# Optimization experiments

Measured on AMD Instinct MI355X. Metric: run time of the kernel, lower is better.

Reference implementation:

```python
import jax, jax.numpy as jnp
import numpy as np

EPS = 1e-5  # batchnorm eps (torch default)


def setup_inputs() -> dict:
    key = jax.random.key(0)
    ks = jax.random.split(key, 16)
    N, E, Din, H, Dout = 100000, 600000, 128, 128, 64
    x = jax.random.normal(ks[0], (N, Din), dtype=jnp.float32)
    edge_index = jax.random.randint(ks[1], (2, E), 0, N, dtype=jnp.int64)
    def lin(k, fan_in, fan_out):
        s = 1.0 / np.sqrt(fan_in)
        return jax.random.uniform(k, (fan_in, fan_out), jnp.float32, -s, s)
    return {
        "x": x,
        "edge_index": edge_index,
        "W1": lin(ks[2], Din, H), "b1": jnp.zeros((H,), jnp.float32),
        "W2": lin(ks[3], H, H),   "b2": jnp.zeros((H,), jnp.float32),
        "W3": lin(ks[4], H, H),   "b3": jnp.zeros((H,), jnp.float32),
        "W4": lin(ks[5], H, Dout),"b4": jnp.zeros((Dout,), jnp.float32),
        "g1": jnp.ones((H,), jnp.float32), "be1": jnp.zeros((H,), jnp.float32),
        "g2": jnp.ones((H,), jnp.float32), "be2": jnp.zeros((H,), jnp.float32),
        "g3": jnp.ones((H,), jnp.float32), "be3": jnp.zeros((H,), jnp.float32),
    }


def _gcn_norm(edge_index, N, dtype):
    # GCNConv default: add self-loops, symmetric normalization D^-1/2 A D^-1/2
    loop = jnp.arange(N, dtype=edge_index.dtype)
    src = jnp.concatenate([edge_index[0], loop])
    dst = jnp.concatenate([edge_index[1], loop])
    deg = jax.ops.segment_sum(jnp.ones_like(src, dtype=dtype), dst, num_segments=N)
    dinv = jax.lax.rsqrt(deg)  # deg >= 1 thanks to self-loops
    norm = dinv[src] * dinv[dst]  # [E+N]
    return src, dst, norm


def _conv(h, W, b, src, dst, norm, N):
    hw = h @ W                      # [N, out]
    msg = hw[src] * norm[:, None]   # gather + scale, [E+N, out]
    return jax.ops.segment_sum(msg, dst, num_segments=N) + b


def _bn(h, gamma, beta):
    # training-mode batchnorm over node dimension (biased variance)
    mu = jnp.mean(h, axis=0)
    var = jnp.mean(jnp.square(h - mu), axis=0)
    return (h - mu) * jax.lax.rsqrt(var + EPS) * gamma + beta


def reference(x, edge_index, W1, b1, W2, b2, W3, b3, W4, b4,
              g1, be1, g2, be2, g3, be3):
    N = x.shape[0]
    src, dst, norm = _gcn_norm(edge_index, N, x.dtype)
    h = jax.nn.relu(_conv(x, W1, b1, src, dst, norm, N))
    h = _bn(h, g1, be1)
    h = jax.nn.relu(_conv(h, W2, b2, src, dst, norm, N))
    h = _bn(h, g2, be2)
    h = jax.nn.relu(_conv(h, W3, b3, src, dst, norm, N))
    h = _bn(h, g3, be3)
    h = jax.nn.relu(_conv(h, W4, b4, src, dst, norm, N))
    return h
```

## Files before the change

kernel.cpp:

```cpp
#include <hip/hip_runtime.h>

#define BN_EPS 1e-5f

using bfrag = __attribute__((ext_vector_type(8))) short;
using f32x4 = __attribute__((ext_vector_type(4))) float;

__device__ inline float bf2f(unsigned int h16) {
    union { unsigned int u; float f; } v; v.u = h16 << 16; return v.f;
}
__device__ inline unsigned short f2bf(float f) {
    union { float f; unsigned int u; } v; v.f = f;
    unsigned int u = v.u;
    u += 0x7fffu + ((u >> 16) & 1u);
    return (unsigned short)(u >> 16);
}
__device__ inline void unpack8(uint4 u, float* f) {
    f[0] = bf2f(u.x & 0xffffu); f[1] = bf2f(u.x >> 16);
    f[2] = bf2f(u.y & 0xffffu); f[3] = bf2f(u.y >> 16);
    f[4] = bf2f(u.z & 0xffffu); f[5] = bf2f(u.z >> 16);
    f[6] = bf2f(u.w & 0xffffu); f[7] = bf2f(u.w >> 16);
}


__global__ void count_kernel(const int* __restrict__ ei, int E, int* __restrict__ cnt) {
    int e = blockIdx.x * blockDim.x + threadIdx.x;
    if (e < E) atomicAdd(&cnt[ei[E + e]], 1);
}

__global__ void dinv_kernel(const int* __restrict__ cnt, float* __restrict__ dinv, int N) {
    int i = blockIdx.x * blockDim.x + threadIdx.x;
    if (i < N) dinv[i] = rsqrtf((float)(cnt[i] + 1));
}

__global__ __launch_bounds__(1024) void scan_blocks(const int* __restrict__ cnt,
                                                    int* __restrict__ rowptr,
                                                    int* __restrict__ bsum, int N) {
    __shared__ int sh[1024];
    int t = threadIdx.x;
    int i = blockIdx.x * 1024 + t;
    int v = (i < N) ? cnt[i] : 0;
    sh[t] = v;
    __syncthreads();
    for (int off = 1; off < 1024; off <<= 1) {
        int x = (t >= off) ? sh[t - off] : 0;
        __syncthreads();
        sh[t] += x;
        __syncthreads();
    }
    if (i < N) rowptr[i] = sh[t] - v;
    if (t == 1023) bsum[blockIdx.x] = sh[1023];
}

__global__ void scan_carry(const int* __restrict__ bsum, int* __restrict__ boff, int nblk) {
    if (threadIdx.x == 0 && blockIdx.x == 0) {
        int run = 0;
        for (int b = 0; b < nblk; ++b) { int v = bsum[b]; boff[b] = run; run += v; }
        boff[nblk] = run;
    }
}

__global__ void scan_add(int* __restrict__ rowptr, const int* __restrict__ boff,
                         int* __restrict__ cursor, int N, int nblk) {
    int i = blockIdx.x * blockDim.x + threadIdx.x;
    if (i < N) {
        int v = rowptr[i] + boff[i >> 10];
        rowptr[i] = v;
        cursor[i] = v;
    }
    if (i == 0) rowptr[N] = boff[nblk];
}

__global__ void fill_kernel(const int* __restrict__ ei, int E, int* __restrict__ cursor,
                            const float* __restrict__ dinv, int* __restrict__ eidx,
                            float* __restrict__ enorm) {
    int e = blockIdx.x * blockDim.x + threadIdx.x;
    if (e < E) {
        int s = ei[e], d = ei[E + e];
        int p = atomicAdd(&cursor[d], 1);
        eidx[p]  = s;
        enorm[p] = dinv[s] * dinv[d];
    }
}

__global__ void s_kernel(const int* __restrict__ rowptr, const float* __restrict__ enorm,
                         const float* __restrict__ dinv, float* __restrict__ sarr, int N) {
    int i = blockIdx.x * blockDim.x + threadIdx.x;
    if (i < N) {
        float a = dinv[i] * dinv[i];
        int j1 = rowptr[i + 1];
        for (int j = rowptr[i]; j < j1; ++j) a += enorm[j];
        sarr[i] = a;
    }
}


template <bool HASBN>
__global__ __launch_bounds__(256) void prep_kernel(const float* __restrict__ W, int COLS,
                                                   const float* __restrict__ stats,
                                                   const float* __restrict__ g,
                                                   const float* __restrict__ be, float invN,
                                                   unsigned short* __restrict__ Wt,
                                                   float* __restrict__ cvec) {
    __shared__ float sc[128], sh[128];
    int tid = threadIdx.x;
    if (tid < 128) {
        if (HASBN) {
            float mu  = stats[tid] * invN;
            float var = stats[128 + tid] * invN - mu * mu;
            float rs  = rsqrtf(var + BN_EPS);
            float s   = rs * g[tid];
            sc[tid] = s;
            sh[tid] = be[tid] - mu * s;
        } else { sc[tid] = 1.f; sh[tid] = 0.f; }
    }
    __syncthreads();
    int total = 128 * COLS;
    for (int idx = blockIdx.x * 256 + tid; idx < total; idx += gridDim.x * 256) {
        int k = idx / COLS, j = idx % COLS;
        Wt[j * 128 + k] = f2bf(sc[k] * W[idx]);
    }
    if (blockIdx.x == 0 && tid < COLS) {
        float a = 0.f;
        if (HASBN)
            for (int k = 0; k < 128; ++k) a += sh[k] * W[k * COLS + tid];
        cvec[tid] = a;
    }
}


template <int COLS, bool IN_F32>
__global__ __launch_bounds__(256) void gemm_mfma(const void* __restrict__ Hin,
                                                 const unsigned short* __restrict__ Wt,
                                                 unsigned short* __restrict__ out, int N) {
    __shared__ unsigned short Hs[64][136];
    const int tid  = threadIdx.x;
    const int row0 = blockIdx.x * 64;

    if (IN_F32) {
        const float* H = (const float*)Hin;
#pragma unroll
        for (int it = 0; it < 8; ++it) {
            int idx = it * 256 + tid;
            int r = idx >> 5, c4 = (idx & 31) * 4;
            float4 v = {0.f, 0.f, 0.f, 0.f};
            if (row0 + r < N) v = *(const float4*)(H + (size_t)(row0 + r) * 128 + c4);
            Hs[r][c4 + 0] = f2bf(v.x); Hs[r][c4 + 1] = f2bf(v.y);
            Hs[r][c4 + 2] = f2bf(v.z); Hs[r][c4 + 3] = f2bf(v.w);
        }
    } else {
        const unsigned short* H = (const unsigned short*)Hin;
#pragma unroll
        for (int it = 0; it < 4; ++it) {
            int idx = it * 256 + tid;
            int r = idx >> 4, c8 = (idx & 15) * 8;
            uint4 v = {0u, 0u, 0u, 0u};
            if (row0 + r < N) v = *(const uint4*)(H + (size_t)(row0 + r) * 128 + c8);
            *(uint4*)&Hs[r][c8] = v;
        }
    }
    __syncthreads();

    const int lane = tid & 63, wave = tid >> 6;
    const int arow = lane & 15, kg = lane >> 4;
    const int r0   = wave * 16;

    bfrag af[4];
#pragma unroll
    for (int kc = 0; kc < 4; ++kc) af[kc] = *(const bfrag*)&Hs[r0 + arow][kc * 32 + kg * 8];

    constexpr int NT = COLS / 16;
    f32x4 acc[NT];
#pragma unroll
    for (int nt = 0; nt < NT; ++nt) acc[nt] = (f32x4){0.f, 0.f, 0.f, 0.f};

#pragma unroll
    for (int nt = 0; nt < NT; ++nt) {
        const unsigned short* wp = Wt + (size_t)(nt * 16 + arow) * 128 + kg * 8;
#pragma unroll
        for (int kc = 0; kc < 4; ++kc) {
            bfrag bf = *(const bfrag*)(wp + kc * 32);
            acc[nt] = __builtin_amdgcn_mfma_f32_16x16x32_bf16(af[kc], bf, acc[nt], 0, 0, 0);
        }
    }
    __syncthreads();

#pragma unroll
    for (int nt = 0; nt < NT; ++nt) {
        int col = nt * 16 + arow;
#pragma unroll
        for (int r = 0; r < 4; ++r)
            Hs[r0 + kg * 4 + r][col] = f2bf(acc[nt][r]);
    }
    __syncthreads();

    constexpr int CH = COLS / 8;
    for (int idx = tid; idx < 64 * CH; idx += 256) {
        int r = idx / CH, c8 = (idx % CH) * 8;
        if (row0 + r < N)
            *(uint4*)(out + (size_t)(row0 + r) * COLS + c8) = *(const uint4*)&Hs[r][c8];
    }
}


template <int F, bool STATS, bool HASC, typename TOUT>
__global__ __launch_bounds__(256) void agg_kernel(const unsigned short* __restrict__ HW,
                                                  const int* __restrict__ rowptr,
                                                  const int* __restrict__ eidx,
                                                  const float* __restrict__ enorm,
                                                  const float* __restrict__ dinv,
                                                  const float* __restrict__ sarr,
                                                  const float* __restrict__ cvec,
                                                  const float* __restrict__ bias,
                                                  TOUT* __restrict__ out,
                                                  float* __restrict__ stats, int N) {
    constexpr int TPR = F / 8;
    constexpr int RPB = 256 / TPR;
    const int tid = threadIdx.x;
    const int lr  = tid / TPR;
    const int j8  = (tid % TPR) * 8;

    float b8[8], c8[8];
#pragma unroll
    for (int k = 0; k < 8; ++k) b8[k] = bias[j8 + k];
    if (HASC) {
#pragma unroll
        for (int k = 0; k < 8; ++k) c8[k] = cvec[j8 + k];
    }

    float ssum[8], ssq[8];
#pragma unroll
    for (int k = 0; k < 8; ++k) { ssum[k] = 0.f; ssq[k] = 0.f; }

    for (int base = blockIdx.x * RPB; base < N; base += gridDim.x * RPB) {
        int row = base + lr;
        if (row < N) {
            float di = dinv[row];
            float w0 = di * di;
            float acc[8], v[8];
            uint4 u = *(const uint4*)(HW + (size_t)row * F + j8);
            unpack8(u, v);
#pragma unroll
            for (int k = 0; k < 8; ++k) acc[k] = w0 * v[k];
            int j0 = rowptr[row], j1 = rowptr[row + 1];
            for (int j = j0; j < j1; ++j) {
                int   s = eidx[j];
                float w = enorm[j];
                uint4 gu = *(const uint4*)(HW + (size_t)s * F + j8);
                unpack8(gu, v);
#pragma unroll
                for (int k = 0; k < 8; ++k) acc[k] += w * v[k];
            }
            if (HASC) {
                float sv = sarr[row];
#pragma unroll
                for (int k = 0; k < 8; ++k) acc[k] += c8[k] * sv;
            }
#pragma unroll
            for (int k = 0; k < 8; ++k) acc[k] = fmaxf(acc[k] + b8[k], 0.f);

            if constexpr (sizeof(TOUT) == 2) {
                unsigned int w0b = (unsigned int)f2bf(acc[0]) | ((unsigned int)f2bf(acc[1]) << 16);
                unsigned int w1b = (unsigned int)f2bf(acc[2]) | ((unsigned int)f2bf(acc[3]) << 16);
                unsigned int w2b = (unsigned int)f2bf(acc[4]) | ((unsigned int)f2bf(acc[5]) << 16);
                unsigned int w3b = (unsigned int)f2bf(acc[6]) | ((unsigned int)f2bf(acc[7]) << 16);
                uint4 o = {w0b, w1b, w2b, w3b};
                *(uint4*)((unsigned short*)out + (size_t)row * F + j8) = o;
            } else {
                float4 o0 = {acc[0], acc[1], acc[2], acc[3]};
                float4 o1 = {acc[4], acc[5], acc[6], acc[7]};
                *(float4*)((float*)out + (size_t)row * F + j8)     = o0;
                *(float4*)((float*)out + (size_t)row * F + j8 + 4) = o1;
            }
            if (STATS) {
#pragma unroll
                for (int k = 0; k < 8; ++k) {
                    ssum[k] += acc[k];
                    ssq[k]  += acc[k] * acc[k];
                }
            }
        }
    }

    if constexpr (STATS) {
        __shared__ float red[RPB][F];
#pragma unroll
        for (int k = 0; k < 8; ++k) red[lr][j8 + k] = ssum[k];
        __syncthreads();
        if (tid < F) {
            float a = 0.f;
#pragma unroll
            for (int r = 0; r < RPB; ++r) a += red[r][tid];
            atomicAdd(&stats[tid], a);
        }
        __syncthreads();
#pragma unroll
        for (int k = 0; k < 8; ++k) red[lr][j8 + k] = ssq[k];
        __syncthreads();
        if (tid < F) {
            float a = 0.f;
#pragma unroll
            for (int r = 0; r < RPB; ++r) a += red[r][tid];
            atomicAdd(&stats[F + tid], a);
        }
    }
}


extern "C" void kernel_launch(void* const* d_in, const int* in_sizes, int n_in,
                              void* d_out, int out_size, void* d_ws, size_t ws_size,
                              hipStream_t stream) {
    const float* x  = (const float*)d_in[0];
    const int*   ei = (const int*)d_in[1];
    const float* W1 = (const float*)d_in[2];  const float* b1 = (const float*)d_in[3];
    const float* W2 = (const float*)d_in[4];  const float* b2 = (const float*)d_in[5];
    const float* W3 = (const float*)d_in[6];  const float* b3 = (const float*)d_in[7];
    const float* W4 = (const float*)d_in[8];  const float* b4 = (const float*)d_in[9];
    const float* g1 = (const float*)d_in[10]; const float* be1 = (const float*)d_in[11];
    const float* g2 = (const float*)d_in[12]; const float* be2 = (const float*)d_in[13];
    const float* g3 = (const float*)d_in[14]; const float* be3 = (const float*)d_in[15];

    const int N = in_sizes[0] / 128;
    const int E = in_sizes[1] / 2;
    const int nblk = (N + 1023) / 1024;

    size_t off = 0;
    char* ws = (char*)d_ws;
    auto alloc = [&](size_t bytes) -> void* {
        void* p = ws + off;
        off += (bytes + 255) & ~(size_t)255;
        return p;
    };
    int*   cnt    = (int*)alloc((size_t)N * 4);
    float* dinv   = (float*)alloc((size_t)N * 4);
    int*   rowptr = (int*)alloc((size_t)(N + 1) * 4);
    int*   cursor = (int*)alloc((size_t)N * 4);
    int*   bsum   = (int*)alloc((size_t)nblk * 4);
    int*   boff   = (int*)alloc((size_t)(nblk + 1) * 4);
    int*   eidx   = (int*)alloc((size_t)E * 4);
    float* enorm  = (float*)alloc((size_t)E * 4);
    float* sarr   = (float*)alloc((size_t)N * 4);
    float* stats  = (float*)alloc(256 * 4);
    unsigned short* Wt = (unsigned short*)alloc(128 * 128 * 2);
    float* cvec   = (float*)alloc(128 * 4);
    unsigned short* hA  = (unsigned short*)alloc((size_t)N * 128 * 2);
    unsigned short* hwB = (unsigned short*)alloc((size_t)N * 128 * 2);
    (void)ws_size; (void)n_in; (void)out_size;

    const int TB = 256;
    const int gE = (E + TB - 1) / TB;
    const int gN = (N + TB - 1) / TB;

    hipMemsetAsync(cnt, 0, (size_t)N * 4, stream);
    count_kernel<<<gE, TB, 0, stream>>>(ei, E, cnt);
    dinv_kernel<<<gN, TB, 0, stream>>>(cnt, dinv, N);
    scan_blocks<<<nblk, 1024, 0, stream>>>(cnt, rowptr, bsum, N);
    scan_carry<<<1, 1, 0, stream>>>(bsum, boff, nblk);
    scan_add<<<gN, TB, 0, stream>>>(rowptr, boff, cursor, N, nblk);
    fill_kernel<<<gE, TB, 0, stream>>>(ei, E, cursor, dinv, eidx, enorm);
    s_kernel<<<gN, TB, 0, stream>>>(rowptr, enorm, dinv, sarr, N);

    const int gG  = (N + 63) / 64;
    const int gA  = 2048;
    const float invN = 1.0f / (float)N;

    prep_kernel<false><<<8, 256, 0, stream>>>(W1, 128, nullptr, nullptr, nullptr, 0.f, Wt, cvec);
    gemm_mfma<128, true><<<gG, 256, 0, stream>>>(x, Wt, hwB, N);
    hipMemsetAsync(stats, 0, 256 * 4, stream);
    agg_kernel<128, true, false, unsigned short><<<gA, 256, 0, stream>>>(
        hwB, rowptr, eidx, enorm, dinv, sarr, cvec, b1, hA, stats, N);

    prep_kernel<true><<<8, 256, 0, stream>>>(W2, 128, stats, g1, be1, invN, Wt, cvec);
    gemm_mfma<128, false><<<gG, 256, 0, stream>>>(hA, Wt, hwB, N);
    hipMemsetAsync(stats, 0, 256 * 4, stream);
    agg_kernel<128, true, true, unsigned short><<<gA, 256, 0, stream>>>(
        hwB, rowptr, eidx, enorm, dinv, sarr, cvec, b2, hA, stats, N);

    prep_kernel<true><<<8, 256, 0, stream>>>(W3, 128, stats, g2, be2, invN, Wt, cvec);
    gemm_mfma<128, false><<<gG, 256, 0, stream>>>(hA, Wt, hwB, N);
    hipMemsetAsync(stats, 0, 256 * 4, stream);
    agg_kernel<128, true, true, unsigned short><<<gA, 256, 0, stream>>>(
        hwB, rowptr, eidx, enorm, dinv, sarr, cvec, b3, hA, stats, N);

    prep_kernel<true><<<8, 256, 0, stream>>>(W4, 64, stats, g3, be3, invN, Wt, cvec);
    gemm_mfma<64, false><<<gG, 256, 0, stream>>>(hA, Wt, hwB, N);
    agg_kernel<64, false, true, float><<<gA, 256, 0, stream>>>(
        hwB, rowptr, eidx, enorm, dinv, sarr, cvec, b4, (float*)d_out, nullptr, N);
}
```

Before: 517.2 us.

## Pack edge index and norm, load cooperatively with shuffles, prefetch gathers

Merges the CSR column indices and edge norms into one int2 array, so each edge's source and weight arrive in a single 8-byte load. In the aggregation kernel, the threads sharing a row each load one packed edge and broadcast it with wave shuffles, instead of every thread reloading the same index and weight. The gather loop is software-pipelined so the next neighbour's feature row is fetched before the current one is accumulated. Bias and cvec are now read inside the loop instead of being cached in registers, which trades extra loads for lower register pressure. The shuffle scheme assumes the threads of a row are contiguous within a 64-lane wave.

New measurement: 490.8 us. 5.1% less time.

```diff
diff --git a/kernel.cpp b/kernel.cpp
--- a/kernel.cpp
+++ b/kernel.cpp
@@ -71,24 +71,23 @@
 }
 
 __global__ void fill_kernel(const int* __restrict__ ei, int E, int* __restrict__ cursor,
-                            const float* __restrict__ dinv, int* __restrict__ eidx,
-                            float* __restrict__ enorm) {
+                            const float* __restrict__ dinv, int2* __restrict__ epack) {
     int e = blockIdx.x * blockDim.x + threadIdx.x;
     if (e < E) {
         int s = ei[e], d = ei[E + e];
         int p = atomicAdd(&cursor[d], 1);
-        eidx[p]  = s;
-        enorm[p] = dinv[s] * dinv[d];
-    }
-}
-
-__global__ void s_kernel(const int* __restrict__ rowptr, const float* __restrict__ enorm,
+        float nrm = dinv[s] * dinv[d];
+        epack[p] = make_int2(s, __float_as_int(nrm));
+    }
+}
+
+__global__ void s_kernel(const int* __restrict__ rowptr, const int2* __restrict__ epack,
                          const float* __restrict__ dinv, float* __restrict__ sarr, int N) {
     int i = blockIdx.x * blockDim.x + threadIdx.x;
     if (i < N) {
         float a = dinv[i] * dinv[i];
         int j1 = rowptr[i + 1];
-        for (int j = rowptr[i]; j < j1; ++j) a += enorm[j];
+        for (int j = rowptr[i]; j < j1; ++j) a += __int_as_float(epack[j].y);
         sarr[i] = a;
     }
 }
@@ -205,8 +204,7 @@
 template <int F, bool STATS, bool HASC, typename TOUT>
 __global__ __launch_bounds__(256) void agg_kernel(const unsigned short* __restrict__ HW,
                                                   const int* __restrict__ rowptr,
-                                                  const int* __restrict__ eidx,
-                                                  const float* __restrict__ enorm,
+                                                  const int2* __restrict__ epack,
                                                   const float* __restrict__ dinv,
                                                   const float* __restrict__ sarr,
                                                   const float* __restrict__ cvec,
@@ -217,19 +215,15 @@
     constexpr int RPB = 256 / TPR;
     const int tid = threadIdx.x;
     const int lr  = tid / TPR;
-    const int j8  = (tid % TPR) * 8;
-
-    float b8[8], c8[8];
-#pragma unroll
-    for (int k = 0; k < 8; ++k) b8[k] = bias[j8 + k];
-    if (HASC) {
-#pragma unroll
-        for (int k = 0; k < 8; ++k) c8[k] = cvec[j8 + k];
-    }
+    const int fo  = tid % TPR;
+    const int j8  = fo * 8;
+    const int lanebase = (tid & 63) & ~(TPR - 1);
 
     float ssum[8], ssq[8];
-#pragma unroll
-    for (int k = 0; k < 8; ++k) { ssum[k] = 0.f; ssq[k] = 0.f; }
+    if (STATS) {
+#pragma unroll
+        for (int k = 0; k < 8; ++k) { ssum[k] = 0.f; ssq[k] = 0.f; }
+    }
 
     for (int base = blockIdx.x * RPB; base < N; base += gridDim.x * RPB) {
         int row = base + lr;
@@ -241,22 +235,34 @@
             unpack8(u, v);
 #pragma unroll
             for (int k = 0; k < 8; ++k) acc[k] = w0 * v[k];
-            int j0 = rowptr[row], j1 = rowptr[row + 1];
-            for (int j = j0; j < j1; ++j) {
-                int   s = eidx[j];
-                float w = enorm[j];
-                uint4 gu = *(const uint4*)(HW + (size_t)s * F + j8);
-                unpack8(gu, v);
-#pragma unroll
-                for (int k = 0; k < 8; ++k) acc[k] += w * v[k];
+
+            const int j0 = rowptr[row], j1 = rowptr[row + 1];
+            for (int jb = j0; jb < j1; jb += TPR) {
+                int myj = jb + fo;
+                int2 ep = (myj < j1) ? epack[myj] : make_int2(0, 0);
+                int cnt = min(j1 - jb, TPR);
+                int   s0 = __shfl(ep.x, lanebase);
+                float g0 = __int_as_float(__shfl(ep.y, lanebase));
+                uint4 G0 = *(const uint4*)(HW + (size_t)s0 * F + j8);
+                for (int t = 0; t < cnt; ++t) {
+                    int tn = (t + 1 < cnt) ? t + 1 : t;
+                    int   s1 = __shfl(ep.x, lanebase + tn);
+                    float g1 = __int_as_float(__shfl(ep.y, lanebase + tn));
+                    uint4 G1 = *(const uint4*)(HW + (size_t)s1 * F + j8);
+                    unpack8(G0, v);
+#pragma unroll
+                    for (int k = 0; k < 8; ++k) acc[k] += g0 * v[k];
+                    G0 = G1; g0 = g1;
+                }
             }
+
             if (HASC) {
                 float sv = sarr[row];
 #pragma unroll
-                for (int k = 0; k < 8; ++k) acc[k] += c8[k] * sv;
+                for (int k = 0; k < 8; ++k) acc[k] += cvec[j8 + k] * sv;
             }
 #pragma unroll
-            for (int k = 0; k < 8; ++k) acc[k] = fmaxf(acc[k] + b8[k], 0.f);
+            for (int k = 0; k < 8; ++k) acc[k] = fmaxf(acc[k] + bias[j8 + k], 0.f);
 
             if constexpr (sizeof(TOUT) == 2) {
                 unsigned int w0b = (unsigned int)f2bf(acc[0]) | ((unsigned int)f2bf(acc[1]) << 16);
@@ -336,8 +342,7 @@
     int*   cursor = (int*)alloc((size_t)N * 4);
     int*   bsum   = (int*)alloc((size_t)nblk * 4);
     int*   boff   = (int*)alloc((size_t)(nblk + 1) * 4);
-    int*   eidx   = (int*)alloc((size_t)E * 4);
-    float* enorm  = (float*)alloc((size_t)E * 4);
+    int2*  epack  = (int2*)alloc((size_t)E * 8);
     float* sarr   = (float*)alloc((size_t)N * 4);
     float* stats  = (float*)alloc(256 * 4);
     unsigned short* Wt = (unsigned short*)alloc(128 * 128 * 2);
@@ -356,8 +361,8 @@
     scan_blocks<<<nblk, 1024, 0, stream>>>(cnt, rowptr, bsum, N);
     scan_carry<<<1, 1, 0, stream>>>(bsum, boff, nblk);
     scan_add<<<gN, TB, 0, stream>>>(rowptr, boff, cursor, N, nblk);
-    fill_kernel<<<gE, TB, 0, stream>>>(ei, E, cursor, dinv, eidx, enorm);
-    s_kernel<<<gN, TB, 0, stream>>>(rowptr, enorm, dinv, sarr, N);
+    fill_kernel<<<gE, TB, 0, stream>>>(ei, E, cursor, dinv, epack);
+    s_kernel<<<gN, TB, 0, stream>>>(rowptr, epack, dinv, sarr, N);
 
     const int gG  = (N + 63) / 64;
     const int gA  = 2048;
@@ -367,22 +372,22 @@
     gemm_mfma<128, true><<<gG, 256, 0, stream>>>(x, Wt, hwB, N);
     hipMemsetAsync(stats, 0, 256 * 4, stream);
     agg_kernel<128, true, false, unsigned short><<<gA, 256, 0, stream>>>(
-        hwB, rowptr, eidx, enorm, dinv, sarr, cvec, b1, hA, stats, N);
+        hwB, rowptr, epack, dinv, sarr, cvec, b1, hA, stats, N);
 
     prep_kernel<true><<<8, 256, 0, stream>>>(W2, 128, stats, g1, be1, invN, Wt, cvec);
     gemm_mfma<128, false><<<gG, 256, 0, stream>>>(hA, Wt, hwB, N);
     hipMemsetAsync(stats, 0, 256 * 4, stream);
     agg_kernel<128, true, true, unsigned short><<<gA, 256, 0, stream>>>(
-        hwB, rowptr, eidx, enorm, dinv, sarr, cvec, b2, hA, stats, N);
+        hwB, rowptr, epack, dinv, sarr, cvec, b2, hA, stats, N);
 
     prep_kernel<true><<<8, 256, 0, stream>>>(W3, 128, stats, g2, be2, invN, Wt, cvec);
     gemm_mfma<128, false><<<gG, 256, 0, stream>>>(hA, Wt, hwB, N);
     hipMemsetAsync(stats, 0, 256 * 4, stream);
     agg_kernel<128, true, true, unsigned short><<<gA, 256, 0, stream>>>(
-        hwB, rowptr, eidx, enorm, dinv, sarr, cvec, b3, hA, stats, N);
+        hwB, rowptr, epack, dinv, sarr, cvec, b3, hA, stats, N);
 
     prep_kernel<true><<<8, 256, 0, stream>>>(W4, 64, stats, g3, be3, invN, Wt, cvec);
     gemm_mfma<64, false><<<gG, 256, 0, stream>>>(hA, Wt, hwB, N);
     agg_kernel<64, false, true, float><<<gA, 256, 0, stream>>>(
-        hwB, rowptr, eidx, enorm, dinv, sarr, cvec, b4, (float*)d_out, nullptr, N);
-}
+        hwB, rowptr, epack, dinv, sarr, cvec, b4, (float*)d_out, nullptr, N);
+}
```

## Pack CSR edges with self-loops and software-pipeline gathers over 4-row groups

Applied to the files above, without the earlier changes.

Edge source index and normalization are packed into one int2 array, and self-loops are inserted into the CSR so the aggregation sees a single uniform edge stream. The aggregation kernel now gives each thread group 4 consecutive rows and walks their combined edge range with a double-buffered, 8-deep prefetch of edge records and feature gathers, flushing a row whenever the row boundary is crossed. This is meant to raise memory-level parallelism on the irregular gathers and cut per-row loop overhead. In exchange it adds register pressure, a larger grid without grid-stride looping, and more complex boundary handling.

New measurement: 461.3 us. 10.8% less time.

```diff
diff --git a/kernel.cpp b/kernel.cpp
--- a/kernel.cpp
+++ b/kernel.cpp
@@ -19,6 +19,12 @@
     f[2] = bf2f(u.y & 0xffffu); f[3] = bf2f(u.y >> 16);
     f[4] = bf2f(u.z & 0xffffu); f[5] = bf2f(u.z >> 16);
     f[6] = bf2f(u.w & 0xffffu); f[7] = bf2f(u.w >> 16);
+}
+__device__ inline void fma8(uint4 G, float w, float* acc) {
+    float v[8];
+    unpack8(G, v);
+#pragma unroll
+    for (int k = 0; k < 8; ++k) acc[k] += w * v[k];
 }
 
 
@@ -38,7 +44,7 @@
     __shared__ int sh[1024];
     int t = threadIdx.x;
     int i = blockIdx.x * 1024 + t;
-    int v = (i < N) ? cnt[i] : 0;
+    int v = (i < N) ? cnt[i] + 1 : 0;
     sh[t] = v;
     __syncthreads();
     for (int off = 1; off < 1024; off <<= 1) {
@@ -71,24 +77,33 @@
 }
 
 __global__ void fill_kernel(const int* __restrict__ ei, int E, int* __restrict__ cursor,
-                            const float* __restrict__ dinv, int* __restrict__ eidx,
-                            float* __restrict__ enorm) {
+                            const float* __restrict__ dinv, int2* __restrict__ epack) {
     int e = blockIdx.x * blockDim.x + threadIdx.x;
     if (e < E) {
         int s = ei[e], d = ei[E + e];
         int p = atomicAdd(&cursor[d], 1);
-        eidx[p]  = s;
-        enorm[p] = dinv[s] * dinv[d];
-    }
-}
-
-__global__ void s_kernel(const int* __restrict__ rowptr, const float* __restrict__ enorm,
-                         const float* __restrict__ dinv, float* __restrict__ sarr, int N) {
+        float nrm = dinv[s] * dinv[d];
+        epack[p] = make_int2(s, __float_as_int(nrm));
+    }
+}
+
+__global__ void self_kernel(int N, int* __restrict__ cursor, const float* __restrict__ dinv,
+                            int2* __restrict__ epack) {
     int i = blockIdx.x * blockDim.x + threadIdx.x;
     if (i < N) {
-        float a = dinv[i] * dinv[i];
+        int p = atomicAdd(&cursor[i], 1);
+        float w = dinv[i] * dinv[i];
+        epack[p] = make_int2(i, __float_as_int(w));
+    }
+}
+
+__global__ void s_kernel(const int* __restrict__ rowptr, const int2* __restrict__ epack,
+                         float* __restrict__ sarr, int N) {
+    int i = blockIdx.x * blockDim.x + threadIdx.x;
+    if (i < N) {
+        float a = 0.f;
         int j1 = rowptr[i + 1];
-        for (int j = rowptr[i]; j < j1; ++j) a += enorm[j];
+        for (int j = rowptr[i]; j < j1; ++j) a += __int_as_float(epack[j].y);
         sarr[i] = a;
     }
 }
@@ -202,104 +217,158 @@
 }
 
 
-template <int F, bool STATS, bool HASC, typename TOUT>
+template <int F, bool STATS, bool HASC, typename TOUT, int RG>
 __global__ __launch_bounds__(256) void agg_kernel(const unsigned short* __restrict__ HW,
                                                   const int* __restrict__ rowptr,
-                                                  const int* __restrict__ eidx,
-                                                  const float* __restrict__ enorm,
-                                                  const float* __restrict__ dinv,
+                                                  const int2* __restrict__ epack,
                                                   const float* __restrict__ sarr,
                                                   const float* __restrict__ cvec,
                                                   const float* __restrict__ bias,
                                                   TOUT* __restrict__ out,
                                                   float* __restrict__ stats, int N) {
-    constexpr int TPR = F / 8;
-    constexpr int RPB = 256 / TPR;
+    constexpr int TPR  = F / 8;
+    constexpr int NGRP = 256 / TPR;
     const int tid = threadIdx.x;
-    const int lr  = tid / TPR;
+    const int grp = tid / TPR;
     const int j8  = (tid % TPR) * 8;
-
-    float b8[8], c8[8];
-#pragma unroll
-    for (int k = 0; k < 8; ++k) b8[k] = bias[j8 + k];
-    if (HASC) {
-#pragma unroll
-        for (int k = 0; k < 8; ++k) c8[k] = cvec[j8 + k];
-    }
+    const int r0  = (blockIdx.x * NGRP + grp) * RG;
 
     float ssum[8], ssq[8];
-#pragma unroll
-    for (int k = 0; k < 8; ++k) { ssum[k] = 0.f; ssq[k] = 0.f; }
-
-    for (int base = blockIdx.x * RPB; base < N; base += gridDim.x * RPB) {
-        int row = base + lr;
-        if (row < N) {
-            float di = dinv[row];
-            float w0 = di * di;
-            float acc[8], v[8];
-            uint4 u = *(const uint4*)(HW + (size_t)row * F + j8);
-            unpack8(u, v);
-#pragma unroll
-            for (int k = 0; k < 8; ++k) acc[k] = w0 * v[k];
-            int j0 = rowptr[row], j1 = rowptr[row + 1];
-            for (int j = j0; j < j1; ++j) {
-                int   s = eidx[j];
-                float w = enorm[j];
-                uint4 gu = *(const uint4*)(HW + (size_t)s * F + j8);
-                unpack8(gu, v);
-#pragma unroll
-                for (int k = 0; k < 8; ++k) acc[k] += w * v[k];
-            }
-            if (HASC) {
-                float sv = sarr[row];
-#pragma unroll
-                for (int k = 0; k < 8; ++k) acc[k] += c8[k] * sv;
-            }
-#pragma unroll
-            for (int k = 0; k < 8; ++k) acc[k] = fmaxf(acc[k] + b8[k], 0.f);
-
-            if constexpr (sizeof(TOUT) == 2) {
-                unsigned int w0b = (unsigned int)f2bf(acc[0]) | ((unsigned int)f2bf(acc[1]) << 16);
-                unsigned int w1b = (unsigned int)f2bf(acc[2]) | ((unsigned int)f2bf(acc[3]) << 16);
-                unsigned int w2b = (unsigned int)f2bf(acc[4]) | ((unsigned int)f2bf(acc[5]) << 16);
-                unsigned int w3b = (unsigned int)f2bf(acc[6]) | ((unsigned int)f2bf(acc[7]) << 16);
-                uint4 o = {w0b, w1b, w2b, w3b};
-                *(uint4*)((unsigned short*)out + (size_t)row * F + j8) = o;
-            } else {
-                float4 o0 = {acc[0], acc[1], acc[2], acc[3]};
-                float4 o1 = {acc[4], acc[5], acc[6], acc[7]};
-                *(float4*)((float*)out + (size_t)row * F + j8)     = o0;
-                *(float4*)((float*)out + (size_t)row * F + j8 + 4) = o1;
-            }
-            if (STATS) {
-#pragma unroll
-                for (int k = 0; k < 8; ++k) {
-                    ssum[k] += acc[k];
-                    ssq[k]  += acc[k] * acc[k];
-                }
-            }
-        }
+    if (STATS) {
+#pragma unroll
+        for (int k = 0; k < 8; ++k) { ssum[k] = 0.f; ssq[k] = 0.f; }
+    }
+
+    if (r0 < N) {
+        float b8[8], c8[8];
+#pragma unroll
+        for (int k = 0; k < 8; ++k) b8[k] = bias[j8 + k];
+        if (HASC) {
+#pragma unroll
+            for (int k = 0; k < 8; ++k) c8[k] = cvec[j8 + k];
+        }
+
+        const int e0 = rowptr[r0];
+        int bound = rowptr[min(r0 + 1, N)];
+        int bnd2  = rowptr[min(r0 + 2, N)];
+        int bnd3  = rowptr[min(r0 + 3, N)];
+        int bnd4  = rowptr[min(r0 + 4, N)];
+        const int eend = bnd4;
+        float sv = 0.f, sv2 = 0.f, sv3 = 0.f, sv4 = 0.f;
+        if (HASC) {
+            sv  = sarr[r0];
+            sv2 = sarr[min(r0 + 1, N - 1)];
+            sv3 = sarr[min(r0 + 2, N - 1)];
+            sv4 = sarr[min(r0 + 3, N - 1)];
+        }
+        int r = r0;
+
+        float acc[8];
+#pragma unroll
+        for (int k = 0; k < 8; ++k) acc[k] = 0.f;
+
+#define FLUSH()                                                               \
+    do {                                                                      \
+        if (HASC) {                                                           \
+            _Pragma("unroll") for (int k = 0; k < 8; ++k) acc[k] += c8[k] * sv; \
+        }                                                                     \
+        _Pragma("unroll") for (int k = 0; k < 8; ++k)                         \
+            acc[k] = fmaxf(acc[k] + b8[k], 0.f);                              \
+        if constexpr (sizeof(TOUT) == 2) {                                    \
+            unsigned int p0 = (unsigned int)f2bf(acc[0]) | ((unsigned int)f2bf(acc[1]) << 16); \
+            unsigned int p1 = (unsigned int)f2bf(acc[2]) | ((unsigned int)f2bf(acc[3]) << 16); \
+            unsigned int p2 = (unsigned int)f2bf(acc[4]) | ((unsigned int)f2bf(acc[5]) << 16); \
+            unsigned int p3 = (unsigned int)f2bf(acc[6]) | ((unsigned int)f2bf(acc[7]) << 16); \
+            uint4 o = {p0, p1, p2, p3};                                       \
+            *(uint4*)((unsigned short*)out + (size_t)r * F + j8) = o;         \
+        } else {                                                              \
+            float4 o0 = {acc[0], acc[1], acc[2], acc[3]};                     \
+            float4 o1 = {acc[4], acc[5], acc[6], acc[7]};                     \
+            *(float4*)((float*)out + (size_t)r * F + j8)     = o0;            \
+            *(float4*)((float*)out + (size_t)r * F + j8 + 4) = o1;            \
+        }                                                                     \
+        if (STATS) {                                                          \
+            _Pragma("unroll") for (int k = 0; k < 8; ++k) {                   \
+                ssum[k] += acc[k];                                            \
+                ssq[k]  += acc[k] * acc[k];                                   \
+            }                                                                 \
+        }                                                                     \
+        _Pragma("unroll") for (int k = 0; k < 8; ++k) acc[k] = 0.f;           \
+        sv = sv2; sv2 = sv3; sv3 = sv4;                                       \
+        bound = bnd2; bnd2 = bnd3; bnd3 = bnd4;                               \
+    } while (0)
+
+#define EPLOAD(ss, ww, ii)                                                    \
+    do { int _i = (ii);                                                       \
+        if (_i < eend) { int2 _e = epack[_i];                                 \
+            ss = _e.x; ww = __int_as_float(_e.y); }                           \
+    } while (0)
+
+#define GISS(G, gw, ss, ww)                                                   \
+    do { G = *(const uint4*)(HW + (size_t)(ss) * F + j8); gw = (ww); } while (0)
+
+#define CONS1(G, gw, ii)                                                      \
+    do { int _c = (ii);                                                       \
+        if (_c < eend) {                                                      \
+            if (_c >= bound) { FLUSH(); ++r; }                                \
+            fma8(G, gw, acc);                                                 \
+        }                                                                     \
+    } while (0)
+
+        int sA0 = 0, sA1 = 0, sA2 = 0, sA3 = 0, sB0 = 0, sB1 = 0, sB2 = 0, sB3 = 0;
+        float wA0 = 0, wA1 = 0, wA2 = 0, wA3 = 0, wB0 = 0, wB1 = 0, wB2 = 0, wB3 = 0;
+        uint4 GA0 = {}, GA1 = {}, GA2 = {}, GA3 = {}, GB0 = {}, GB1 = {}, GB2 = {}, GB3 = {};
+        float ga0 = 0, ga1 = 0, ga2 = 0, ga3 = 0, gb0 = 0, gb1 = 0, gb2 = 0, gb3 = 0;
+
+        EPLOAD(sA0, wA0, e0 + 0); EPLOAD(sA1, wA1, e0 + 1);
+        EPLOAD(sA2, wA2, e0 + 2); EPLOAD(sA3, wA3, e0 + 3);
+        EPLOAD(sB0, wB0, e0 + 4); EPLOAD(sB1, wB1, e0 + 5);
+        EPLOAD(sB2, wB2, e0 + 6); EPLOAD(sB3, wB3, e0 + 7);
+        GISS(GA0, ga0, sA0, wA0); GISS(GA1, ga1, sA1, wA1);
+        GISS(GA2, ga2, sA2, wA2); GISS(GA3, ga3, sA3, wA3);
+
+        for (int b = e0; b < eend; b += 8) {
+            EPLOAD(sA0, wA0, b + 8);  EPLOAD(sA1, wA1, b + 9);
+            EPLOAD(sA2, wA2, b + 10); EPLOAD(sA3, wA3, b + 11);
+            GISS(GB0, gb0, sB0, wB0); GISS(GB1, gb1, sB1, wB1);
+            GISS(GB2, gb2, sB2, wB2); GISS(GB3, gb3, sB3, wB3);
+            CONS1(GA0, ga0, b + 0); CONS1(GA1, ga1, b + 1);
+            CONS1(GA2, ga2, b + 2); CONS1(GA3, ga3, b + 3);
+
+            EPLOAD(sB0, wB0, b + 12); EPLOAD(sB1, wB1, b + 13);
+            EPLOAD(sB2, wB2, b + 14); EPLOAD(sB3, wB3, b + 15);
+            GISS(GA0, ga0, sA0, wA0); GISS(GA1, ga1, sA1, wA1);
+            GISS(GA2, ga2, sA2, wA2); GISS(GA3, ga3, sA3, wA3);
+            CONS1(GB0, gb0, b + 4); CONS1(GB1, gb1, b + 5);
+            CONS1(GB2, gb2, b + 6); CONS1(GB3, gb3, b + 7);
+        }
+        FLUSH();
+
+#undef FLUSH
+#undef EPLOAD
+#undef GISS
+#undef CONS1
     }
 
     if constexpr (STATS) {
-        __shared__ float red[RPB][F];
-#pragma unroll
-        for (int k = 0; k < 8; ++k) red[lr][j8 + k] = ssum[k];
+        __shared__ float red[NGRP][F];
+#pragma unroll
+        for (int k = 0; k < 8; ++k) red[grp][j8 + k] = ssum[k];
         __syncthreads();
         if (tid < F) {
             float a = 0.f;
 #pragma unroll
-            for (int r = 0; r < RPB; ++r) a += red[r][tid];
+            for (int g = 0; g < NGRP; ++g) a += red[g][tid];
             atomicAdd(&stats[tid], a);
         }
         __syncthreads();
 #pragma unroll
-        for (int k = 0; k < 8; ++k) red[lr][j8 + k] = ssq[k];
+        for (int k = 0; k < 8; ++k) red[grp][j8 + k] = ssq[k];
         __syncthreads();
         if (tid < F) {
             float a = 0.f;
 #pragma unroll
-            for (int r = 0; r < RPB; ++r) a += red[r][tid];
+            for (int g = 0; g < NGRP; ++g) a += red[g][tid];
             atomicAdd(&stats[F + tid], a);
         }
     }
@@ -336,8 +405,7 @@
     int*   cursor = (int*)alloc((size_t)N * 4);
     int*   bsum   = (int*)alloc((size_t)nblk * 4);
     int*   boff   = (int*)alloc((size_t)(nblk + 1) * 4);
-    int*   eidx   = (int*)alloc((size_t)E * 4);
-    float* enorm  = (float*)alloc((size_t)E * 4);
+    int2*  epack  = (int2*)alloc((size_t)(E + N) * 8);
     float* sarr   = (float*)alloc((size_t)N * 4);
     float* stats  = (float*)alloc(256 * 4);
     unsigned short* Wt = (unsigned short*)alloc(128 * 128 * 2);
@@ -356,33 +424,35 @@
     scan_blocks<<<nblk, 1024, 0, stream>>>(cnt, rowptr, bsum, N);
     scan_carry<<<1, 1, 0, stream>>>(bsum, boff, nblk);
     scan_add<<<gN, TB, 0, stream>>>(rowptr, boff, cursor, N, nblk);
-    fill_kernel<<<gE, TB, 0, stream>>>(ei, E, cursor, dinv, eidx, enorm);
-    s_kernel<<<gN, TB, 0, stream>>>(rowptr, enorm, dinv, sarr, N);
-
-    const int gG  = (N + 63) / 64;
-    const int gA  = 2048;
+    fill_kernel<<<gE, TB, 0, stream>>>(ei, E, cursor, dinv, epack);
+    self_kernel<<<gN, TB, 0, stream>>>(N, cursor, dinv, epack);
+    s_kernel<<<gN, TB, 0, stream>>>(rowptr, epack, sarr, N);
+
+    const int gG    = (N + 63) / 64;
+    const int gA128 = (N + 63) / 64;
+    const int gA64  = (N + 127) / 128;
     const float invN = 1.0f / (float)N;
 
     prep_kernel<false><<<8, 256, 0, stream>>>(W1, 128, nullptr, nullptr, nullptr, 0.f, Wt, cvec);
     gemm_mfma<128, true><<<gG, 256, 0, stream>>>(x, Wt, hwB, N);
     hipMemsetAsync(stats, 0, 256 * 4, stream);
-    agg_kernel<128, true, false, unsigned short><<<gA, 256, 0, stream>>>(
-        hwB, rowptr, eidx, enorm, dinv, sarr, cvec, b1, hA, stats, N);
+    agg_kernel<128, true, false, unsigned short, 4><<<gA128, 256, 0, stream>>>(
+        hwB, rowptr, epack, sarr, cvec, b1, hA, stats, N);
 
     prep_kernel<true><<<8, 256, 0, stream>>>(W2, 128, stats, g1, be1, invN, Wt, cvec);
     gemm_mfma<128, false><<<gG, 256, 0, stream>>>(hA, Wt, hwB, N);
     hipMemsetAsync(stats, 0, 256 * 4, stream);
-    agg_kernel<128, true, true, unsigned short><<<gA, 256, 0, stream>>>(
-        hwB, rowptr, eidx, enorm, dinv, sarr, cvec, b2, hA, stats, N);
+    agg_kernel<128, true, true, unsigned short, 4><<<gA128, 256, 0, stream>>>(
+        hwB, rowptr, epack, sarr, cvec, b2, hA, stats, N);
 
     prep_kernel<true><<<8, 256, 0, stream>>>(W3, 128, stats, g2, be2, invN, Wt, cvec);
     gemm_mfma<128, false><<<gG, 256, 0, stream>>>(hA, Wt, hwB, N);
     hipMemsetAsync(stats, 0, 256 * 4, stream);
-    agg_kernel<128, true, true, unsigned short><<<gA, 256, 0, stream>>>(
-        hwB, rowptr, eidx, enorm, dinv, sarr, cvec, b3, hA, stats, N);
+    agg_kernel<128, true, true, unsigned short, 4><<<gA128, 256, 0, stream>>>(
+        hwB, rowptr, epack, sarr, cvec, b3, hA, stats, N);
 
     prep_kernel<true><<<8, 256, 0, stream>>>(W4, 64, stats, g3, be3, invN, Wt, cvec);
     gemm_mfma<64, false><<<gG, 256, 0, stream>>>(hA, Wt, hwB, N);
-    agg_kernel<64, false, true, float><<<gA, 256, 0, stream>>>(
-        hwB, rowptr, eidx, enorm, dinv, sarr, cvec, b4, (float*)d_out, nullptr, N);
-}
+    agg_kernel<64, false, true, float, 4><<<gA64, 256, 0, stream>>>(
+        hwB, rowptr, epack, sarr, cvec, b4, (float*)d_out, nullptr, N);
+}
```
